# Kernel optimization log

Hardware: AMD Instinct MI355X
Metric: run time of the kernel (lower is better)

## Reference

```python
import jax, jax.numpy as jnp
import numpy as np

HIDDEN = 2048
HEAD_DIM = 128
Q_HEAD = 16
KV_HEAD = 2
MAX_TOKEN = 4096
THETA = 10000
B = 1
S = 2048
SCALER = 1.0 / np.sqrt(HEAD_DIM)


def make_pos_emb():
    # Faithful port of ROPEEmbedding.create_embedding
    i = np.repeat(np.arange(HEAD_DIM // 2), 2)            # [D]
    freq = np.power(float(THETA), -i * 2.0 / HEAD_DIM)    # [D]
    t = np.einsum('i,j->ij', freq, np.arange(MAX_TOKEN, dtype=np.float64))  # [D, T]
    cos = np.cos(t)
    sin = np.sin(t)
    sin[0::2] *= -1.0                                      # negate even rows (even dim indices)
    pe = np.concatenate([cos, sin], axis=0).T              # [T, 2D]
    return jnp.asarray(pe, jnp.float32)


def _flip_pairs(x):
    # swap adjacent pairs along last dim: (x0,x1,x2,x3,..) -> (x1,x0,x3,x2,..)
    b, h, s, d = x.shape
    return x.reshape(b, h, s, d // 2, 2)[..., ::-1].reshape(b, h, s, d)


def _apply_rope(x, pos_emb):
    # x: [B, H, S, D]; pos_emb: [max_token, 2D]
    s = x.shape[2]
    pe = pos_emb[:s]                     # [S, 2D]
    cos = pe[:, :HEAD_DIM]               # [S, D]
    sin = pe[:, HEAD_DIM:]               # [S, D] (signed)
    return x * cos + _flip_pairs(x) * sin


def setup_inputs() -> dict:
    key = jax.random.key(0)
    ks = jax.random.split(key, 5)
    qkv_out = (Q_HEAD + 2 * KV_HEAD) * HEAD_DIM  # 2560
    lim_qkv = 1.0 / np.sqrt(HIDDEN)
    lim_o = 1.0 / np.sqrt(Q_HEAD * HEAD_DIM)
    x = jax.random.normal(ks[0], (B, S, HIDDEN), dtype=jnp.float32)
    w_qkv = jax.random.uniform(ks[1], (qkv_out, HIDDEN), jnp.float32, -lim_qkv, lim_qkv)
    b_qkv = jax.random.uniform(ks[2], (qkv_out,), jnp.float32, -lim_qkv, lim_qkv)
    w_o = jax.random.uniform(ks[3], (HIDDEN, Q_HEAD * HEAD_DIM), jnp.float32, -lim_o, lim_o)
    b_o = jax.random.uniform(ks[4], (HIDDEN,), jnp.float32, -lim_o, lim_o)
    # causal additive mask, as typically passed to this module
    neg = jnp.float32(-1e9)
    attention_mask = jnp.where(
        jnp.tril(jnp.ones((S, S), dtype=bool)), jnp.float32(0.0), neg
    )[None, None, :, :]
    pos_emb = make_pos_emb()
    return {"tensor": x, "attention_mask": attention_mask, "w_qkv": w_qkv,
            "b_qkv": b_qkv, "w_o": w_o, "b_o": b_o, "pos_emb": pos_emb}


def reference(tensor, attention_mask, w_qkv, b_qkv, w_o, b_o, pos_emb):
    b, s, _ = tensor.shape
    qkv = tensor @ w_qkv.T + b_qkv                        # [B, S, 2560]
    dq = HEAD_DIM * Q_HEAD
    dkv = HEAD_DIM * KV_HEAD
    q = qkv[..., :dq].reshape(b, s, Q_HEAD, HEAD_DIM)
    k = qkv[..., dq:dq + dkv].reshape(b, s, KV_HEAD, HEAD_DIM)
    v = qkv[..., dq + dkv:].reshape(b, s, KV_HEAD, HEAD_DIM)
    scale = Q_HEAD // KV_HEAD
    k = jnp.repeat(k, scale, axis=2)                      # [B, S, Q_HEAD, D]
    v = jnp.repeat(v, scale, axis=2)
    q = q.transpose(0, 2, 1, 3)                           # [B, H, S, D]
    k = k.transpose(0, 2, 1, 3)
    v = v.transpose(0, 2, 1, 3)
    q = _apply_rope(q, pos_emb)
    k = _apply_rope(k, pos_emb)
    scores = jnp.einsum('bhqd,bhkd->bhqk', q, k) * SCALER
    scores = scores + attention_mask
    attn = jax.nn.softmax(scores, axis=-1)
    out = jnp.einsum('bhqk,bhkd->bhqd', attn, v)          # [B, H, S, D]
    out = out.transpose(0, 2, 1, 3).reshape(b, s, Q_HEAD * HEAD_DIM)
    return out @ w_o.T + b_o
```

## Files before the change

kernel.cpp:

```cpp
#include <hip/hip_runtime.h>
#include <stdint.h>

#define SQ 2048
#define DH 128
#define SCALER 0.08838834764831845f

typedef float f32x4 __attribute__((ext_vector_type(4)));
typedef short s16x8 __attribute__((ext_vector_type(8)));

__device__ __forceinline__ short f2bf(float f) {
  uint32_t x = __float_as_uint(f);
  uint32_t r = (x + 0x7fffu + ((x >> 16) & 1u)) >> 16;
  return (short)(r & 0xffffu);
}

__device__ __forceinline__ void mfma16(f32x4& d, s16x8 a, s16x8 b) {
  asm("v_mfma_f32_16x16x32_bf16 %0, %1, %2, %0" : "+v"(d) : "v"(a), "v"(b));
}

__device__ __forceinline__ void gload16(const void* g, void* l) {
  __builtin_amdgcn_global_load_lds(
      (__attribute__((address_space(1))) void*)const_cast<void*>(g),
      (__attribute__((address_space(3))) void*)l, 16, 0, 0);
}

__global__ __launch_bounds__(256) void cvt_bf16(const float* __restrict__ in,
                                                short* __restrict__ out, int n8) {
  int i = blockIdx.x * 256 + threadIdx.x;
  if (i >= n8) return;
  const float4* p = (const float4*)in + (size_t)i * 2;
  float4 a = p[0], b = p[1];
  s16x8 o;
  o[0] = f2bf(a.x); o[1] = f2bf(a.y); o[2] = f2bf(a.z); o[3] = f2bf(a.w);
  o[4] = f2bf(b.x); o[5] = f2bf(b.y); o[6] = f2bf(b.z); o[7] = f2bf(b.w);
  *((s16x8*)out + i) = o;
}

__global__ __launch_bounds__(256) void gemm_bt_bias(
    const short* __restrict__ A, const short* __restrict__ B,
    const float* __restrict__ bias, float* __restrict__ C,
    int M, int N, int K) {
  __shared__ __align__(16) short As[128 * 64];
  __shared__ __align__(16) short Bs[128 * 64];
  const int t = threadIdx.x;
  const int l = t & 63, w = t >> 6;
  const int wr = w >> 1, wc = w & 1;
  const int lr = l & 15, lk = l >> 4;
  const int m0 = blockIdx.y * 128, n0 = blockIdx.x * 128;

  f32x4 acc[4][4] = {};

  for (int kt = 0; kt < K; kt += 64) {
    const short* ga = A + (size_t)m0 * K + kt;
    const short* gb = B + (size_t)n0 * K + kt;
#pragma unroll
    for (int i = 0; i < 4; ++i) {
      int j = i * 256 + t;
      int lbase = (i * 256 + (t & ~63)) << 4;
      gload16(ga + (size_t)(j >> 3) * K + ((j & 7) << 3), (char*)As + lbase);
      gload16(gb + (size_t)(j >> 3) * K + ((j & 7) << 3), (char*)Bs + lbase);
    }
    __syncthreads();
#pragma unroll
    for (int ks = 0; ks < 2; ++ks) {
      s16x8 af[4], bg[4];
#pragma unroll
      for (int i = 0; i < 4; ++i) {
        af[i] = *(const s16x8*)(As + (wr * 64 + i * 16 + lr) * 64 + ks * 32 + lk * 8);
        bg[i] = *(const s16x8*)(Bs + (wc * 64 + i * 16 + lr) * 64 + ks * 32 + lk * 8);
      }
#pragma unroll
      for (int mi = 0; mi < 4; ++mi)
#pragma unroll
        for (int ni = 0; ni < 4; ++ni)
          mfma16(acc[mi][ni], af[mi], bg[ni]);
    }
    __syncthreads();
  }
#pragma unroll
  for (int mi = 0; mi < 4; ++mi) {
    int row = m0 + wr * 64 + mi * 16 + lk * 4;
#pragma unroll
    for (int ni = 0; ni < 4; ++ni) {
      int col = n0 + wc * 64 + ni * 16 + lr;
      float bv = bias[col];
#pragma unroll
      for (int r = 0; r < 4; ++r)
        C[(size_t)(row + r) * N + col] = acc[mi][ni][r] + bv;
    }
  }
}

__global__ __launch_bounds__(256) void rope_split(
    const float* __restrict__ qkv, const float* __restrict__ pe,
    short* __restrict__ qws, short* __restrict__ kws, short* __restrict__ vtws) {
  const int s = blockIdx.x;
  const int t = threadIdx.x;
  const float* row = qkv + (size_t)s * 2560;
  const float* per = pe + (size_t)s * 256;
#pragma unroll
  for (int i = 0; i < 5; ++i) {
    int p = t + i * 256;
    int c0 = p * 2;
    float x0 = row[c0], x1 = row[c0 + 1];
    int d0 = c0 & 127;
    if (c0 < 2048) {
      int hq = c0 >> 7;
      float cc0 = per[d0], cc1 = per[d0 + 1], ss0 = per[128 + d0], ss1 = per[128 + d0 + 1];
      float y0 = (x0 * cc0 + x1 * ss0) * SCALER;
      float y1 = (x1 * cc1 + x0 * ss1) * SCALER;
      size_t off = ((size_t)hq * SQ + s) * DH + d0;
      uint32_t u = (uint32_t)(uint16_t)f2bf(y0) | ((uint32_t)(uint16_t)f2bf(y1) << 16);
      *(uint32_t*)(qws + off) = u;
    } else if (c0 < 2304) {
      int hk = (c0 - 2048) >> 7;
      float cc0 = per[d0], cc1 = per[d0 + 1], ss0 = per[128 + d0], ss1 = per[128 + d0 + 1];
      float y0 = x0 * cc0 + x1 * ss0;
      float y1 = x1 * cc1 + x0 * ss1;
      size_t off = (size_t)hk * SQ * DH + (size_t)s * DH + (size_t)((((d0 >> 3) ^ (s & 15)) << 3) + (d0 & 7));
      uint32_t u = (uint32_t)(uint16_t)f2bf(y0) | ((uint32_t)(uint16_t)f2bf(y1) << 16);
      *(uint32_t*)(kws + off) = u;
    } else {
      int hk = (c0 - 2304) >> 7;
      size_t base = (size_t)hk * DH * SQ;
      int sl = s & 63;
      int d1 = d0 + 1;
      size_t off0 = base + (size_t)d0 * SQ + (s >> 6) * 64 + ((((sl >> 3) ^ (d0 & 7)) << 3) + (sl & 7));
      size_t off1 = base + (size_t)d1 * SQ + (s >> 6) * 64 + ((((sl >> 3) ^ (d1 & 7)) << 3) + (sl & 7));
      vtws[off0] = f2bf(x0);
      vtws[off1] = f2bf(x1);
    }
  }
}

__global__ __launch_bounds__(256) void attn_fwd(
    const short* __restrict__ qws, const short* __restrict__ kws,
    const short* __restrict__ vtws, short* __restrict__ attnws) {
  __shared__ __align__(16) short Ks[2][64 * 128];
  __shared__ __align__(16) short Vt[2][128 * 64];
  __shared__ __align__(16) short Ps[4][16 * 72];

  const int bx = blockIdx.x;
  const int h = bx & 15;
  const int qb = 31 - (bx >> 4);
  const int hk = h >> 3;
  const int t = threadIdx.x, l = t & 63, w = t >> 6;
  const int lr = l & 15, lk = l >> 4;

  s16x8 qf[4];
  {
    const short* qbase = qws + ((size_t)h * SQ + (size_t)qb * 64 + w * 16) * DH;
#pragma unroll
    for (int kd = 0; kd < 4; ++kd)
      qf[kd] = *(const s16x8*)(qbase + (size_t)lr * DH + kd * 32 + lk * 8);
  }

  f32x4 o[8] = {};
  f32x4 m_, l_;
#pragma unroll
  for (int r = 0; r < 4; ++r) { m_[r] = -1e30f; l_[r] = 0.f; }

  const short* gkh = kws + (size_t)hk * SQ * DH;
  const short* gvh = vtws + (size_t)hk * DH * SQ;

#define STAGE(buf, kb)                                                          \
  {                                                                             \
    const short* gk = gkh + (size_t)(kb)*64 * DH;                               \
    const short* gv = gvh + (size_t)(kb)*64;                                    \
    _Pragma("unroll") for (int i = 0; i < 4; ++i) {                             \
      int j = i * 256 + t;                                                      \
      int lbase = (i * 256 + (t & ~63)) << 4;                                   \
      gload16(gk + (size_t)(j >> 4) * DH + ((j & 15) << 3),                     \
              (char*)Ks[buf] + lbase);                                          \
      gload16(gv + (size_t)(j >> 3) * SQ + ((j & 7) << 3),                      \
              (char*)Vt[buf] + lbase);                                          \
    }                                                                           \
  }

  STAGE(0, 0);
  __syncthreads();

  const int row_base = w * 16;

  for (int kb = 0; kb <= qb; ++kb) {
    const int cur = kb & 1;
    if (kb < qb) STAGE(cur ^ 1, kb + 1);

    f32x4 sc_[4] = {};
#pragma unroll
    for (int kd = 0; kd < 4; ++kd) {
      s16x8 bfr[4];
#pragma unroll
      for (int nt = 0; nt < 4; ++nt) {
        int krow = nt * 16 + lr;
        int slot = (kd * 4 + lk) ^ lr;
        bfr[nt] = *(const s16x8*)(Ks[cur] + krow * 128 + slot * 8);
      }
#pragma unroll
      for (int nt = 0; nt < 4; ++nt)
        mfma16(sc_[nt], qf[kd], bfr[nt]);
    }
    if (kb == qb) {
#pragma unroll
      for (int nt = 0; nt < 4; ++nt)
#pragma unroll
        for (int r = 0; r < 4; ++r) {
          int col = nt * 16 + lr;
          int row = row_base + lk * 4 + r;
          if (col > row) sc_[nt][r] = -1e30f;
        }
    }
    {
      f32x4 rm;
#pragma unroll
      for (int r = 0; r < 4; ++r)
        rm[r] = fmaxf(fmaxf(sc_[0][r], sc_[1][r]), fmaxf(sc_[2][r], sc_[3][r]));
#pragma unroll
      for (int off = 1; off < 16; off <<= 1)
#pragma unroll
        for (int r = 0; r < 4; ++r) rm[r] = fmaxf(rm[r], __shfl_xor(rm[r], off, 16));
      f32x4 mn, scl, rs;
#pragma unroll
      for (int r = 0; r < 4; ++r) {
        mn[r] = fmaxf(m_[r], rm[r]);
        scl[r] = __expf(m_[r] - mn[r]);
        rs[r] = 0.f;
      }
#pragma unroll
      for (int nt = 0; nt < 4; ++nt)
#pragma unroll
        for (int r = 0; r < 4; ++r) {
          sc_[nt][r] = __expf(sc_[nt][r] - mn[r]);
          rs[r] += sc_[nt][r];
        }
#pragma unroll
      for (int off = 1; off < 16; off <<= 1)
#pragma unroll
        for (int r = 0; r < 4; ++r) rs[r] += __shfl_xor(rs[r], off, 16);
#pragma unroll
      for (int r = 0; r < 4; ++r) {
        l_[r] = l_[r] * scl[r] + rs[r];
        m_[r] = mn[r];
      }
#pragma unroll
      for (int dt = 0; dt < 8; ++dt)
#pragma unroll
        for (int r = 0; r < 4; ++r) o[dt][r] *= scl[r];
      short* ps = (short*)Ps[w];
#pragma unroll
      for (int nt = 0; nt < 4; ++nt)
#pragma unroll
        for (int r = 0; r < 4; ++r)
          ps[(lk * 4 + r) * 72 + nt * 16 + lr] = f2bf(sc_[nt][r]);
    }
    {
      const short* ps = (const short*)Ps[w];
#pragma unroll
      for (int kp = 0; kp < 2; ++kp) {
        s16x8 pa = *(const s16x8*)(ps + lr * 72 + kp * 32 + lk * 8);
#pragma unroll
        for (int dt = 0; dt < 8; ++dt) {
          int drow = dt * 16 + lr;
          int slot = (kp * 4 + lk) ^ (lr & 7);
          s16x8 vb = *(const s16x8*)(Vt[cur] + drow * 64 + slot * 8);
          mfma16(o[dt], pa, vb);
        }
      }
    }
    __syncthreads();
  }
#undef STAGE

#pragma unroll
  for (int dt = 0; dt < 8; ++dt) {
    int col = h * DH + dt * 16 + lr;
#pragma unroll
    for (int r = 0; r < 4; ++r) {
      int srow = qb * 64 + w * 16 + lk * 4 + r;
      float val = o[dt][r] / l_[r];
      attnws[(size_t)srow * 2048 + col] = f2bf(val);
    }
  }
}

extern "C" void kernel_launch(void* const* d_in, const int* in_sizes, int n_in,
                              void* d_out, int out_size, void* d_ws, size_t ws_size,
                              hipStream_t stream) {
  (void)in_sizes; (void)n_in; (void)out_size; (void)ws_size;
  const float* x     = (const float*)d_in[0];
  const float* w_qkv = (const float*)d_in[2];
  const float* b_qkv = (const float*)d_in[3];
  const float* w_o   = (const float*)d_in[4];
  const float* b_o   = (const float*)d_in[5];
  const float* pe    = (const float*)d_in[6];
  float* out = (float*)d_out;

  short* xb     = (short*)d_ws;
  short* wqkvb  = xb + (size_t)2048 * 2048;
  short* wob    = wqkvb + (size_t)2560 * 2048;
  float* qkv    = (float*)(wob + (size_t)2048 * 2048);
  short* qws    = (short*)(qkv + (size_t)2048 * 2560);
  short* kws    = qws + (size_t)16 * 2048 * 128;
  short* vtws   = kws + (size_t)2 * 2048 * 128;
  short* attnws = xb;

  cvt_bf16<<<2048, 256, 0, stream>>>(x, xb, 2048 * 2048 / 8);
  cvt_bf16<<<2560, 256, 0, stream>>>(w_qkv, wqkvb, 2560 * 2048 / 8);
  cvt_bf16<<<2048, 256, 0, stream>>>(w_o, wob, 2048 * 2048 / 8);
  gemm_bt_bias<<<dim3(2560 / 128, 2048 / 128), 256, 0, stream>>>(
      xb, wqkvb, b_qkv, qkv, 2048, 2560, 2048);
  rope_split<<<2048, 256, 0, stream>>>(qkv, pe, qws, kws, vtws);
  attn_fwd<<<512, 256, 0, stream>>>(qws, kws, vtws, attnws);
  gemm_bt_bias<<<dim3(2048 / 128, 2048 / 128), 256, 0, stream>>>(
      attnws, wob, b_o, out, 2048, 2048, 2048);
}
```

Measured before the change: 182.0 us.

## Fuse RoPE and QKV split into QKV GEMM epilogue; reorder attention blocks

Folds the rope_split kernel into the QKV projection GEMM epilogue through a MODE template, so the GEMM writes bf16 rotated Q/K and transposed V straight to their workspaces. This removes the fp32 qkv intermediate round trip and one kernel launch. The epilogue now does scattered 2-byte stores and per-element pos_emb loads, and uses a lane shuffle to fetch each RoPE pair partner. It also changes the attention block order so the second half of blocks handles query blocks in ascending order, and moves attnws so it no longer aliases xb.

```diff
diff --git a/kernel.cpp b/kernel.cpp
--- a/kernel.cpp
+++ b/kernel.cpp
@@ -36,9 +36,12 @@
   *((s16x8*)out + i) = o;
 }
 
+template <int MODE>
 __global__ __launch_bounds__(256) void gemm_bt_bias(
     const short* __restrict__ A, const short* __restrict__ B,
     const float* __restrict__ bias, float* __restrict__ C,
+    const float* __restrict__ pe, short* __restrict__ qws,
+    short* __restrict__ kws, short* __restrict__ vtws,
     int M, int N, int K) {
   __shared__ __align__(16) short As[128 * 64];
   __shared__ __align__(16) short Bs[128 * 64];
@@ -77,6 +80,7 @@
     }
     __syncthreads();
   }
+
 #pragma unroll
   for (int mi = 0; mi < 4; ++mi) {
     int row = m0 + wr * 64 + mi * 16 + lk * 4;
@@ -85,50 +89,34 @@
       int col = n0 + wc * 64 + ni * 16 + lr;
       float bv = bias[col];
 #pragma unroll
-      for (int r = 0; r < 4; ++r)
-        C[(size_t)(row + r) * N + col] = acc[mi][ni][r] + bv;
-    }
-  }
-}
-
-__global__ __launch_bounds__(256) void rope_split(
-    const float* __restrict__ qkv, const float* __restrict__ pe,
-    short* __restrict__ qws, short* __restrict__ kws, short* __restrict__ vtws) {
-  const int s = blockIdx.x;
-  const int t = threadIdx.x;
-  const float* row = qkv + (size_t)s * 2560;
-  const float* per = pe + (size_t)s * 256;
-#pragma unroll
-  for (int i = 0; i < 5; ++i) {
-    int p = t + i * 256;
-    int c0 = p * 2;
-    float x0 = row[c0], x1 = row[c0 + 1];
-    int d0 = c0 & 127;
-    if (c0 < 2048) {
-      int hq = c0 >> 7;
-      float cc0 = per[d0], cc1 = per[d0 + 1], ss0 = per[128 + d0], ss1 = per[128 + d0 + 1];
-      float y0 = (x0 * cc0 + x1 * ss0) * SCALER;
-      float y1 = (x1 * cc1 + x0 * ss1) * SCALER;
-      size_t off = ((size_t)hq * SQ + s) * DH + d0;
-      uint32_t u = (uint32_t)(uint16_t)f2bf(y0) | ((uint32_t)(uint16_t)f2bf(y1) << 16);
-      *(uint32_t*)(qws + off) = u;
-    } else if (c0 < 2304) {
-      int hk = (c0 - 2048) >> 7;
-      float cc0 = per[d0], cc1 = per[d0 + 1], ss0 = per[128 + d0], ss1 = per[128 + d0 + 1];
-      float y0 = x0 * cc0 + x1 * ss0;
-      float y1 = x1 * cc1 + x0 * ss1;
-      size_t off = (size_t)hk * SQ * DH + (size_t)s * DH + (size_t)((((d0 >> 3) ^ (s & 15)) << 3) + (d0 & 7));
-      uint32_t u = (uint32_t)(uint16_t)f2bf(y0) | ((uint32_t)(uint16_t)f2bf(y1) << 16);
-      *(uint32_t*)(kws + off) = u;
-    } else {
-      int hk = (c0 - 2304) >> 7;
-      size_t base = (size_t)hk * DH * SQ;
-      int sl = s & 63;
-      int d1 = d0 + 1;
-      size_t off0 = base + (size_t)d0 * SQ + (s >> 6) * 64 + ((((sl >> 3) ^ (d0 & 7)) << 3) + (sl & 7));
-      size_t off1 = base + (size_t)d1 * SQ + (s >> 6) * 64 + ((((sl >> 3) ^ (d1 & 7)) << 3) + (sl & 7));
-      vtws[off0] = f2bf(x0);
-      vtws[off1] = f2bf(x1);
+      for (int r = 0; r < 4; ++r) {
+        float v = acc[mi][ni][r] + bv;
+        if (MODE == 0) {
+          C[(size_t)(row + r) * N + col] = v;
+        } else {
+          int s = row + r;
+          int d = col & 127;
+          if (n0 < 2048) {
+            float p = __shfl_xor(v, 1);
+            const float* per = pe + (size_t)s * 256;
+            float y = (v * per[d] + p * per[128 + d]) * SCALER;
+            int hq = col >> 7;
+            qws[((size_t)hq * SQ + s) * DH + d] = f2bf(y);
+          } else if (n0 < 2304) {
+            float p = __shfl_xor(v, 1);
+            const float* per = pe + (size_t)s * 256;
+            float y = v * per[d] + p * per[128 + d];
+            int hk = (col - 2048) >> 7;
+            kws[(size_t)hk * SQ * DH + (size_t)s * DH +
+                (size_t)((((d >> 3) ^ (s & 15)) << 3) + (d & 7))] = f2bf(y);
+          } else {
+            int hk = (col - 2304) >> 7;
+            int sl = s & 63;
+            vtws[(size_t)hk * DH * SQ + (size_t)d * SQ + (s >> 6) * 64 +
+                 (size_t)((((sl >> 3) ^ (d & 7)) << 3) + (sl & 7))] = f2bf(v);
+          }
+        }
+      }
     }
   }
 }
@@ -142,7 +130,8 @@
 
   const int bx = blockIdx.x;
   const int h = bx & 15;
-  const int qb = 31 - (bx >> 4);
+  const int i_ = bx >> 4;
+  const int qb = (i_ < 16) ? (31 - i_) : (i_ - 16);
   const int hk = h >> 3;
   const int t = threadIdx.x, l = t & 63, w = t >> 6;
   const int lr = l & 15, lk = l >> 4;
@@ -298,19 +287,17 @@
   short* xb     = (short*)d_ws;
   short* wqkvb  = xb + (size_t)2048 * 2048;
   short* wob    = wqkvb + (size_t)2560 * 2048;
-  float* qkv    = (float*)(wob + (size_t)2048 * 2048);
-  short* qws    = (short*)(qkv + (size_t)2048 * 2560);
+  short* qws    = wob + (size_t)2048 * 2048;
   short* kws    = qws + (size_t)16 * 2048 * 128;
   short* vtws   = kws + (size_t)2 * 2048 * 128;
-  short* attnws = xb;
+  short* attnws = vtws + (size_t)2 * 128 * 2048;
 
   cvt_bf16<<<2048, 256, 0, stream>>>(x, xb, 2048 * 2048 / 8);
   cvt_bf16<<<2560, 256, 0, stream>>>(w_qkv, wqkvb, 2560 * 2048 / 8);
   cvt_bf16<<<2048, 256, 0, stream>>>(w_o, wob, 2048 * 2048 / 8);
-  gemm_bt_bias<<<dim3(2560 / 128, 2048 / 128), 256, 0, stream>>>(
-      xb, wqkvb, b_qkv, qkv, 2048, 2560, 2048);
-  rope_split<<<2048, 256, 0, stream>>>(qkv, pe, qws, kws, vtws);
+  gemm_bt_bias<1><<<dim3(2560 / 128, 2048 / 128), 256, 0, stream>>>(
+      xb, wqkvb, b_qkv, nullptr, pe, qws, kws, vtws, 2048, 2560, 2048);
   attn_fwd<<<512, 256, 0, stream>>>(qws, kws, vtws, attnws);
-  gemm_bt_bias<<<dim3(2048 / 128, 2048 / 128), 256, 0, stream>>>(
-      attnws, wob, b_o, out, 2048, 2048, 2048);
-}
+  gemm_bt_bias<0><<<dim3(2048 / 128, 2048 / 128), 256, 0, stream>>>(
+      attnws, wob, b_o, out, nullptr, nullptr, nullptr, nullptr, 2048, 2048, 2048);
+}
```

Result: slower. 189.5 us (+4.1%).
